# Performance work log

Hardware: AMD Instinct MI355X
Metric: run time of the kernel (lower is better)

Reference implementation:

```python
import jax, jax.numpy as jnp
import numpy as np

D_MODEL = 512
STATE = 128
HALF = STATE // 2
SEQ = 4096
BATCH = 8


def setup_inputs() -> dict:
    key = jax.random.key(0)
    ks = jax.random.split(key, 4)
    u = jax.random.normal(ks[0], (BATCH, SEQ, D_MODEL), dtype=jnp.float32)
    # HiPPO init: Lambda = -0.5 + i*pi*n, n=1..HALF
    n = jnp.arange(1, HALF + 1, dtype=jnp.float32)
    log_Lambda_real = jnp.log(jnp.full((HALF,), 0.5, dtype=jnp.float32))  # log(-real) with real=-0.5
    Lambda_imag = jnp.pi * n
    B_real = jnp.ones((HALF, D_MODEL), dtype=jnp.float32)
    B_imag = jnp.zeros((HALF, D_MODEL), dtype=jnp.float32)
    C_real = jax.random.normal(ks[1], (D_MODEL, HALF), dtype=jnp.float32) / np.sqrt(STATE)
    C_imag = jax.random.normal(ks[2], (D_MODEL, HALF), dtype=jnp.float32) / np.sqrt(STATE)
    D = jax.random.normal(ks[3], (D_MODEL, D_MODEL), dtype=jnp.float32) / np.sqrt(D_MODEL)
    log_Delta = jnp.array([-3.0], dtype=jnp.float32)
    return {
        "u": u,
        "log_Lambda_real": log_Lambda_real,
        "Lambda_imag": Lambda_imag,
        "B_real": B_real,
        "B_imag": B_imag,
        "C_real": C_real,
        "C_imag": C_imag,
        "D": D,
        "log_Delta": log_Delta,
    }


def reference(u, log_Lambda_real, Lambda_imag, B_real, B_imag, C_real, C_imag, D, log_Delta):
    T = u.shape[1]
    Bc = B_real + 1j * B_imag            # (N/2, P) complex
    Cc = C_real + 1j * C_imag            # (P, N/2) complex
    # --- bilinear (Tustin) discretization ---
    Delta = jnp.exp(log_Delta)           # (1,)
    Lambda = -jnp.exp(jnp.clip(log_Lambda_real, -10.0, 10.0)) + 1j * Lambda_imag  # (N/2,)
    denom = 1.0 - (Delta / 2.0) * Lambda
    A_bar = (1.0 + (Delta / 2.0) * Lambda) / denom          # (N/2,)
    B_bar = (Delta / denom)[:, None] * Bc                   # (N/2, P)
    # --- FFT convolution with the SSM kernel k[n,t] = A_bar[n]^t ---
    t_idx = jnp.arange(T)
    k = jnp.exp(jnp.log(A_bar)[:, None] * t_idx[None, :])   # (N/2, T)
    u_c = u.astype(jnp.complex64)
    v = jnp.einsum('np,btp->bnt', B_bar, u_c)               # (B, N/2, T)
    fft_size = 2 * T
    V_f = jnp.fft.fft(v, n=fft_size, axis=-1)
    K_f = jnp.fft.fft(k, n=fft_size, axis=-1)
    conv = jnp.fft.ifft(V_f * K_f[None, :, :], axis=-1)[..., :T]  # (B, N/2, T)
    y = 2.0 * jnp.einsum('pn,bnt->btp', Cc, conv).real      # (B, T, P)
    return y + u @ D.T
```

## Files before the change

kernel.cpp:

```cpp
#include <hip/hip_runtime.h>
#include <hip/hip_bf16.h>
#include <stdint.h>


#define BATCH 8
#define SEQ   4096
#define DMODEL 512
#define HALF  64
#define CHUNK 64
#define NCHUNK (SEQ / CHUNK)

typedef __attribute__((ext_vector_type(8))) short short8;
typedef __attribute__((ext_vector_type(4))) float f32x4;

__device__ __forceinline__ unsigned short f2bf(float f) {
    unsigned int u = __float_as_uint(f);
    u += 0x7fffu + ((u >> 16) & 1u);
    return (unsigned short)(u >> 16);
}

#define GLOAD_LDS16(g, l)                                                    \
    __builtin_amdgcn_global_load_lds(                                        \
        (const __attribute__((address_space(1))) unsigned int*)(g),          \
        (__attribute__((address_space(3))) unsigned int*)(l), 16, 0, 0)


__global__ void k_consts(const float* __restrict__ logLr,
                         const float* __restrict__ Li_in,
                         const float* __restrict__ logDelta,
                         float* __restrict__ sr, float* __restrict__ si,
                         float* __restrict__ ApR, float* __restrict__ ApI) {
    int n = threadIdx.x;
    float Delta = expf(logDelta[0]);
    float llr = fminf(fmaxf(logLr[n], -10.f), 10.f);
    float Lr = -expf(llr);
    float Li = Li_in[n];
    float dr = 1.f - 0.5f * Delta * Lr;
    float di = -0.5f * Delta * Li;
    float dn = dr * dr + di * di;
    float nr = 1.f + 0.5f * Delta * Lr;
    float ni = 0.5f * Delta * Li;
    float Ar = (nr * dr + ni * di) / dn;
    float Ai = (ni * dr - nr * di) / dn;
    sr[n] = Delta * dr / dn;
    si[n] = -Delta * di / dn;
    float pr = 1.f, pi = 0.f;
    for (int k = 0; k <= CHUNK; ++k) {
        ApR[k * HALF + n] = pr;
        ApI[k * HALF + n] = pi;
        float npr = pr * Ar - pi * Ai;
        float npi = pr * Ai + pi * Ar;
        pr = npr; pi = npi;
    }
}

__global__ void k_build_Mv(const float* __restrict__ Br, const float* __restrict__ Bi,
                           const float* __restrict__ sr, const float* __restrict__ si,
                           unsigned short* __restrict__ Mv) {
    int np = blockIdx.x, p = threadIdx.x;
    int n = np & 63;
    float br = Br[n * DMODEL + p], bi = Bi[n * DMODEL + p];
    float v = (np < HALF) ? (sr[n] * br - si[n] * bi)
                          : (si[n] * br + sr[n] * bi);
    Mv[np * DMODEL + p] = f2bf(v);
}

__global__ void k_build_W(const float* __restrict__ Cr, const float* __restrict__ Ci,
                          const float* __restrict__ D, unsigned short* __restrict__ W) {
    int p = blockIdx.x, j = threadIdx.x;
    float v;
    if (j < HALF) v = 2.f * Cr[p * HALF + j];
    else if (j < 2 * HALF) v = -2.f * Ci[p * HALF + (j - HALF)];
    else v = D[p * DMODEL + (j - 2 * HALF)];
    W[p * 640 + j] = f2bf(v);
}


__global__ void k_scanA(const float* __restrict__ V,
                        const float* __restrict__ ApR, const float* __restrict__ ApI,
                        float* __restrict__ E) {
    int tid = threadIdx.x;
    int n = tid & 63;
    int c = ((blockIdx.x & 31) << 1) + (tid >> 6);
    int b = blockIdx.x >> 5;
    float Ar = ApR[HALF + n], Ai = ApI[HALF + n];
    float xr = 0.f, xi = 0.f;
    size_t base = ((size_t)b * SEQ + (size_t)c * CHUNK) * 128 + n;
    for (int tl = 0; tl < CHUNK; ++tl) {
        float vr = V[base], vi = V[base + 64];
        float nxr = Ar * xr - Ai * xi + vr;
        float nxi = Ar * xi + Ai * xr + vi;
        xr = nxr; xi = nxi;
        base += 128;
    }
    int eidx = ((b * NCHUNK + c) * 2) * HALF + n;
    E[eidx] = xr; E[eidx + 64] = xi;
}

__global__ void k_scanB(const float* __restrict__ E, float* __restrict__ Carry,
                        const float* __restrict__ ApR, const float* __restrict__ ApI) {
    int lane = threadIdx.x & 63;
    int wv = threadIdx.x >> 6;
    int b = blockIdx.x;
    for (int n = wv; n < HALF; n += 8) {
        float wr = ApR[CHUNK * HALF + n], wi = ApI[CHUNK * HALF + n];
        int idx = ((b * NCHUNK + lane) * 2) * HALF + n;
        float sR = E[idx], sI = E[idx + 64];
#pragma unroll
        for (int s = 1; s < 64; s <<= 1) {
            float pR = __shfl_up(sR, s, 64);
            float pI = __shfl_up(sI, s, 64);
            if (lane >= s) {
                sR += wr * pR - wi * pI;
                sI += wr * pI + wi * pR;
            }
            float nwr = wr * wr - wi * wi;
            float nwi = 2.f * wr * wi;
            wr = nwr; wi = nwi;
        }
        float cR = __shfl_up(sR, 1, 64);
        float cI = __shfl_up(sI, 1, 64);
        if (lane == 0) { cR = 0.f; cI = 0.f; }
        Carry[idx] = cR; Carry[idx + 64] = cI;
    }
}

template <int WRITE_V, int WRITE_XB>
__global__ void k_scanC(float* __restrict__ V, const float* __restrict__ Carry,
                        const float* __restrict__ ApR, const float* __restrict__ ApI,
                        unsigned short* __restrict__ Xb) {
    int tid = threadIdx.x;
    int n = tid & 63;
    int c = ((blockIdx.x & 31) << 1) + (tid >> 6);
    int b = blockIdx.x >> 5;
    int cidx = ((b * NCHUNK + c) * 2) * HALF + n;
    float xr = Carry[cidx], xi = Carry[cidx + 64];
    float Ar = ApR[HALF + n], Ai = ApI[HALF + n];
    size_t base = ((size_t)b * SEQ + (size_t)c * CHUNK) * 128 + n;
    for (int tl = 0; tl < CHUNK; ++tl) {
        float vr = V[base], vi = V[base + 64];
        float nxr = Ar * xr - Ai * xi + vr;
        float nxi = Ar * xi + Ai * xr + vi;
        xr = nxr; xi = nxi;
        if (WRITE_XB) { Xb[base] = f2bf(xr); Xb[base + 64] = f2bf(xi); }
        if (WRITE_V)  { V[base] = xr; V[base + 64] = xi; }
        base += 128;
    }
}

__global__ __launch_bounds__(512) void gemm1(const float* __restrict__ U,
                                             const unsigned short* __restrict__ Mv,
                                             float* __restrict__ V,
                                             unsigned short* __restrict__ Ub,
                                             int writeUb) {
    __shared__ __align__(16) unsigned short As[64 * 32];
    __shared__ __align__(16) unsigned short Bs[128 * 32];
    const int tid = threadIdx.x;
    const int lane = tid & 63;
    const int w = tid >> 6;
    const int wm = w >> 2, wn = w & 3;
    const int l15 = lane & 15, l4 = lane >> 4;
    const int row0 = blockIdx.x * 64;
    const int srow = tid >> 3;
    const int sh = (tid & 7) * 4;

    f32x4 acc[2][2];
#pragma unroll
    for (int m = 0; m < 2; ++m)
#pragma unroll
        for (int n = 0; n < 2; ++n) acc[m][n] = (f32x4)(0.f);

    for (int k0 = 0; k0 < DMODEL; k0 += 32) {
        const float4 av = *(const float4*)(U + (size_t)(row0 + srow) * DMODEL + k0 + sh);

        __syncthreads();

        GLOAD_LDS16(Mv + (size_t)(tid >> 2) * DMODEL + k0 + (tid & 3) * 8,
                    &Bs[(w * 64) * 8]);

        uint2 wa;
        wa.x = (unsigned)f2bf(av.x) | ((unsigned)f2bf(av.y) << 16);
        wa.y = (unsigned)f2bf(av.z) | ((unsigned)f2bf(av.w) << 16);
        *(uint2*)&As[srow * 32 + sh] = wa;
        if (writeUb)
            *(uint2*)&Ub[(size_t)(row0 + srow) * DMODEL + k0 + sh] = wa;

        __syncthreads();

        short8 af[2], bf[2];
#pragma unroll
        for (int m = 0; m < 2; ++m)
            af[m] = *(const short8*)&As[(wm * 32 + m * 16 + l15) * 32 + l4 * 8];
#pragma unroll
        for (int n = 0; n < 2; ++n)
            bf[n] = *(const short8*)&Bs[(wn * 32 + n * 16 + l15) * 32 + l4 * 8];
#pragma unroll
        for (int m = 0; m < 2; ++m)
#pragma unroll
            for (int n = 0; n < 2; ++n)
                acc[m][n] = __builtin_amdgcn_mfma_f32_16x16x32_bf16(af[m], bf[n], acc[m][n], 0, 0, 0);
    }

#pragma unroll
    for (int m = 0; m < 2; ++m) {
        int rbase = row0 + wm * 32 + m * 16 + l4 * 4;
#pragma unroll
        for (int n = 0; n < 2; ++n) {
            int col = wn * 32 + n * 16 + l15;
#pragma unroll
            for (int r = 0; r < 4; ++r)
                V[(size_t)(rbase + r) * 128 + col] = acc[m][n][r];
        }
    }
}


#define STAGE_A8(t, q) do {                                                    \
    int c_ = (q) * 512 + tid;                                                  \
    int ct_ = c_ ^ (((c_ >> 5) & 1) << 1);                                     \
    int r_ = (ct_ >> 2) & 255;                                                 \
    int kcol_ = (t) * 64 + (ct_ >> 10) * 32 + (ct_ & 3) * 8;                   \
    const unsigned short* src_ = (kcol_ < 128)                                 \
        ? Xb + (size_t)(row0 + r_) * 128 + kcol_                               \
        : Ub + (size_t)(row0 + r_) * 512 + (kcol_ - 128);                      \
    GLOAD_LDS16(src_, &As[((t) & 1) * 16384 + ((q) * 512 + w * 64) * 8]);      \
} while (0)

#define STAGE_B8(t, q) do {                                                    \
    int c_ = (q) * 512 + tid;                                                  \
    int ct_ = c_ ^ (((c_ >> 5) & 1) << 1);                                     \
    int r_ = (ct_ >> 2) & 255;                                                 \
    int kcol_ = (t) * 64 + (ct_ >> 10) * 32 + (ct_ & 3) * 8;                   \
    GLOAD_LDS16(W + (size_t)(col0 + r_) * 640 + kcol_,                         \
                &Bs[((t) & 1) * 16384 + ((q) * 512 + w * 64) * 8]);            \
} while (0)

#define LDA8(t, mq) do {                                                       \
    _Pragma("unroll") for (int m2_ = 0; m2_ < 4; ++m2_)                        \
    _Pragma("unroll") for (int kh_ = 0; kh_ < 2; ++kh_) {                      \
        int r_ = wm * 128 + ((mq) * 4 + m2_) * 16 + l15;                       \
        int c_ = (l4 * 8) ^ (((r_ >> 3) & 1) << 4);                            \
        af[m2_][kh_] = *(const short8*)                                        \
            &As[((t) & 1) * 16384 + kh_ * 8192 + r_ * 32 + c_];                \
    } } while (0)

#define LDB8(t, nq) do {                                                       \
    _Pragma("unroll") for (int n2_ = 0; n2_ < 2; ++n2_)                        \
    _Pragma("unroll") for (int kh_ = 0; kh_ < 2; ++kh_) {                      \
        int r_ = wn * 64 + ((nq) * 2 + n2_) * 16 + l15;                        \
        int c_ = (l4 * 8) ^ (((r_ >> 3) & 1) << 4);                            \
        bf[n2_][kh_] = *(const short8*)                                        \
            &Bs[((t) & 1) * 16384 + kh_ * 8192 + r_ * 32 + c_];                \
    } } while (0)

#define MFMA8(mq, nq) do {                                                     \
    __builtin_amdgcn_s_setprio(1);                                             \
    _Pragma("unroll") for (int m2_ = 0; m2_ < 4; ++m2_)                        \
    _Pragma("unroll") for (int n2_ = 0; n2_ < 2; ++n2_)                        \
    _Pragma("unroll") for (int kh_ = 0; kh_ < 2; ++kh_)                        \
        acc[(mq) * 4 + m2_][(nq) * 2 + n2_] =                                  \
            __builtin_amdgcn_mfma_f32_16x16x32_bf16(                           \
                af[m2_][kh_], bf[n2_][kh_],                                    \
                acc[(mq) * 4 + m2_][(nq) * 2 + n2_], 0, 0, 0);                 \
    __builtin_amdgcn_s_setprio(0);                                             \
} while (0)

__global__ __launch_bounds__(512) void gemm23_8p(const unsigned short* __restrict__ Xb,
                                                 const unsigned short* __restrict__ Ub,
                                                 const unsigned short* __restrict__ W,
                                                 float* __restrict__ C) {
    __shared__ __align__(16) unsigned short As[2 * 16384];
    __shared__ __align__(16) unsigned short Bs[2 * 16384];
    const int tid = threadIdx.x;
    const int lane = tid & 63;
    const int w = tid >> 6;
    const int wm = w >> 2, wn = w & 3;
    const int l15 = lane & 15, l4 = lane >> 4;

    int lin = blockIdx.y * gridDim.x + blockIdx.x;
    int sw = (lin & 7) * 32 + (lin >> 3);
    const int row0 = (sw & 127) * 256;
    const int col0 = (sw >> 7) * 256;

    f32x4 acc[8][4];
#pragma unroll
    for (int m = 0; m < 8; ++m)
#pragma unroll
        for (int n = 0; n < 4; ++n) acc[m][n] = (f32x4)(0.f);

#pragma unroll
    for (int q = 0; q < 4; ++q) { STAGE_A8(0, q); STAGE_B8(0, q); }
    __syncthreads();

    short8 af[4][2], bf[2][2];
    for (int t = 0; t < 10; ++t) {
        const bool pf = (t < 9);
        LDA8(t, 0); LDB8(t, 0);
        if (pf) { STAGE_A8(t + 1, 0); STAGE_B8(t + 1, 0); }
        __builtin_amdgcn_s_barrier();
        MFMA8(0, 0);
        __builtin_amdgcn_s_barrier();
        LDB8(t, 1);
        if (pf) { STAGE_A8(t + 1, 1); STAGE_B8(t + 1, 1); }
        __builtin_amdgcn_s_barrier();
        MFMA8(0, 1);
        __builtin_amdgcn_s_barrier();
        LDA8(t, 1); LDB8(t, 0);
        if (pf) { STAGE_A8(t + 1, 2); STAGE_B8(t + 1, 2); }
        __builtin_amdgcn_s_barrier();
        MFMA8(1, 0);
        __builtin_amdgcn_s_barrier();
        LDB8(t, 1);
        if (pf) { STAGE_A8(t + 1, 3); STAGE_B8(t + 1, 3); }
        __builtin_amdgcn_s_barrier();
        MFMA8(1, 1);
        __syncthreads();
    }

#pragma unroll
    for (int m = 0; m < 8; ++m) {
        int rbase = row0 + wm * 128 + m * 16 + l4 * 4;
#pragma unroll
        for (int n = 0; n < 4; ++n) {
            int col = col0 + wn * 64 + n * 16 + l15;
#pragma unroll
            for (int r = 0; r < 4; ++r)
                C[(size_t)(rbase + r) * DMODEL + col] = acc[m][n][r];
        }
    }
}

__global__ __launch_bounds__(256) void gemm23_f32a(
    const float* __restrict__ A0, int lda0,
    const float* __restrict__ A1, int lda1,
    const unsigned short* __restrict__ B, int ldb,
    float* __restrict__ C, int ldc, int K, int SPLIT)
{
    __shared__ __align__(16) unsigned short As[128 * 32];
    __shared__ __align__(16) unsigned short Bs[128 * 32];
    const int tid = threadIdx.x;
    const int lane = tid & 63;
    const int w = tid >> 6;
    const int wm = w >> 1, wn = w & 1;
    const int l15 = lane & 15, l4 = lane >> 4;
    const int row0 = blockIdx.x * 128;
    const int col0 = blockIdx.y * 128;
    const int srow = tid >> 1;
    const int sh = (tid & 1) << 4;

    f32x4 acc[4][4];
#pragma unroll
    for (int m = 0; m < 4; ++m)
#pragma unroll
        for (int n = 0; n < 4; ++n) acc[m][n] = (f32x4)(0.f);

    for (int k0 = 0; k0 < K; k0 += 32) {
        const float* ap; int lda, kk;
        if (k0 < SPLIT) { ap = A0; lda = lda0; kk = k0; }
        else { ap = A1; lda = lda1; kk = k0 - SPLIT; }
        const float* ag = ap + (size_t)(row0 + srow) * lda + kk + sh;
        float4 av0 = ((const float4*)ag)[0];
        float4 av1 = ((const float4*)ag)[1];
        float4 av2 = ((const float4*)ag)[2];
        float4 av3 = ((const float4*)ag)[3];

        __syncthreads();

#pragma unroll
        for (int i = 0; i < 2; ++i) {
            int c = i * 256 + w * 64 + lane;
            GLOAD_LDS16(B + (size_t)(col0 + (c >> 2)) * ldb + k0 + (c & 3) * 8,
                        &Bs[(i * 256 + w * 64) * 8]);
        }

        uint4 wa0, wa1;
        wa0.x = (unsigned)f2bf(av0.x) | ((unsigned)f2bf(av0.y) << 16);
        wa0.y = (unsigned)f2bf(av0.z) | ((unsigned)f2bf(av0.w) << 16);
        wa0.z = (unsigned)f2bf(av1.x) | ((unsigned)f2bf(av1.y) << 16);
        wa0.w = (unsigned)f2bf(av1.z) | ((unsigned)f2bf(av1.w) << 16);
        wa1.x = (unsigned)f2bf(av2.x) | ((unsigned)f2bf(av2.y) << 16);
        wa1.y = (unsigned)f2bf(av2.z) | ((unsigned)f2bf(av2.w) << 16);
        wa1.z = (unsigned)f2bf(av3.x) | ((unsigned)f2bf(av3.y) << 16);
        wa1.w = (unsigned)f2bf(av3.z) | ((unsigned)f2bf(av3.w) << 16);
        uint4* adst = (uint4*)&As[srow * 32 + sh];
        adst[0] = wa0; adst[1] = wa1;

        __syncthreads();

        short8 af[4], bf[4];
#pragma unroll
        for (int m = 0; m < 4; ++m)
            af[m] = *(const short8*)&As[(wm * 64 + m * 16 + l15) * 32 + l4 * 8];
#pragma unroll
        for (int n = 0; n < 4; ++n)
            bf[n] = *(const short8*)&Bs[(wn * 64 + n * 16 + l15) * 32 + l4 * 8];
#pragma unroll
        for (int m = 0; m < 4; ++m)
#pragma unroll
            for (int n = 0; n < 4; ++n)
                acc[m][n] = __builtin_amdgcn_mfma_f32_16x16x32_bf16(af[m], bf[n], acc[m][n], 0, 0, 0);
    }

#pragma unroll
    for (int m = 0; m < 4; ++m) {
        int rbase = row0 + wm * 64 + m * 16 + l4 * 4;
#pragma unroll
        for (int n = 0; n < 4; ++n) {
            int col = col0 + wn * 64 + n * 16 + l15;
#pragma unroll
            for (int r = 0; r < 4; ++r)
                C[(size_t)(rbase + r) * ldc + col] = acc[m][n][r];
        }
    }
}


extern "C" void kernel_launch(void* const* d_in, const int* in_sizes, int n_in,
                              void* d_out, int out_size, void* d_ws, size_t ws_size,
                              hipStream_t stream) {
    const float* u      = (const float*)d_in[0];
    const float* logLr  = (const float*)d_in[1];
    const float* Li     = (const float*)d_in[2];
    const float* Br     = (const float*)d_in[3];
    const float* Bi     = (const float*)d_in[4];
    const float* Cr     = (const float*)d_in[5];
    const float* Ci     = (const float*)d_in[6];
    const float* D      = (const float*)d_in[7];
    const float* logDel = (const float*)d_in[8];
    float* out = (float*)d_out;

    const size_t M = (size_t)BATCH * SEQ;
    float* ws    = (float*)d_ws;
    float* V     = ws;
    float* E     = V + M * 128;
    float* Carry = E + 65536;
    float* ApR   = Carry + 65536;
    float* ApI   = ApR + 4160;
    float* sr    = ApI + 4160;
    float* si    = sr + 64;
    unsigned short* Mv = (unsigned short*)(si + 64);
    unsigned short* W  = Mv + 128 * 512;
    unsigned short* Ub = W + 512 * 640;
    unsigned short* Xb = Ub + M * 512;
    const size_t need = (size_t)((char*)(Xb + M * 128) - (char*)ws);
    const int big = (ws_size >= need);

    hipLaunchKernelGGL(k_consts, dim3(1), dim3(64), 0, stream,
                       logLr, Li, logDel, sr, si, ApR, ApI);
    hipLaunchKernelGGL(k_build_Mv, dim3(128), dim3(512), 0, stream, Br, Bi, sr, si, Mv);
    hipLaunchKernelGGL(k_build_W, dim3(512), dim3(640), 0, stream, Cr, Ci, D, W);

    hipLaunchKernelGGL(gemm1, dim3(M / 64), dim3(512), 0, stream, u, Mv, V, Ub, big);

    hipLaunchKernelGGL(k_scanA, dim3(256), dim3(128), 0, stream, V, ApR, ApI, E);
    hipLaunchKernelGGL(k_scanB, dim3(BATCH), dim3(512), 0, stream, E, Carry, ApR, ApI);
    if (big) {
        hipLaunchKernelGGL((k_scanC<0, 1>), dim3(256), dim3(128), 0, stream,
                           V, Carry, ApR, ApI, Xb);
        hipLaunchKernelGGL(gemm23_8p, dim3(M / 256, DMODEL / 256), dim3(512), 0, stream,
                           Xb, Ub, W, out);
    } else {
        hipLaunchKernelGGL((k_scanC<1, 0>), dim3(256), dim3(128), 0, stream,
                           V, Carry, ApR, ApI, (unsigned short*)nullptr);
        hipLaunchKernelGGL(gemm23_f32a, dim3(M / 128, DMODEL / 128), dim3(256), 0, stream,
                           V, 128, u, DMODEL, W, 640, out, DMODEL, 640, 128);
    }
}
```

Measured before the change: 89.37 us.

## Store V in bf16, preload Mv into LDS, restructure gemm23 pipeline, drop fallback

Writes the intermediate V in bf16 instead of fp32, halving the traffic of the gemm1 output and of the scan reads. gemm1 now keeps the whole Mv matrix in LDS with an XOR swizzle, uses 128-row tiles and reads U straight into registers. The gemm23 loop moves from four sub-phases to two k-halves with explicit vmcnt waits so loads overlap the MFMAs. The small-workspace fallback path is removed, so a large workspace is assumed, and rounding V to bf16 before the scan adds precision loss.

```diff
diff --git a/kernel.cpp b/kernel.cpp
--- a/kernel.cpp
+++ b/kernel.cpp
@@ -9,6 +9,7 @@
 #define HALF  64
 #define CHUNK 64
 #define NCHUNK (SEQ / CHUNK)
+#define NT    10
 
 typedef __attribute__((ext_vector_type(8))) short short8;
 typedef __attribute__((ext_vector_type(4))) float f32x4;
@@ -17,6 +18,9 @@
     unsigned int u = __float_as_uint(f);
     u += 0x7fffu + ((u >> 16) & 1u);
     return (unsigned short)(u >> 16);
+}
+__device__ __forceinline__ float bf2f(unsigned short s) {
+    return __uint_as_float((unsigned)s << 16);
 }
 
 #define GLOAD_LDS16(g, l)                                                    \
@@ -76,7 +80,7 @@
 }
 
 
-__global__ void k_scanA(const float* __restrict__ V,
+__global__ void k_scanA(const unsigned short* __restrict__ Vb,
                         const float* __restrict__ ApR, const float* __restrict__ ApI,
                         float* __restrict__ E) {
     int tid = threadIdx.x;
@@ -87,7 +91,7 @@
     float xr = 0.f, xi = 0.f;
     size_t base = ((size_t)b * SEQ + (size_t)c * CHUNK) * 128 + n;
     for (int tl = 0; tl < CHUNK; ++tl) {
-        float vr = V[base], vi = V[base + 64];
+        float vr = bf2f(Vb[base]), vi = bf2f(Vb[base + 64]);
         float nxr = Ar * xr - Ai * xi + vr;
         float nxi = Ar * xi + Ai * xr + vi;
         xr = nxr; xi = nxi;
@@ -125,8 +129,8 @@
     }
 }
 
-template <int WRITE_V, int WRITE_XB>
-__global__ void k_scanC(float* __restrict__ V, const float* __restrict__ Carry,
+__global__ void k_scanC(const unsigned short* __restrict__ Vb,
+                        const float* __restrict__ Carry,
                         const float* __restrict__ ApR, const float* __restrict__ ApI,
                         unsigned short* __restrict__ Xb) {
     int tid = threadIdx.x;
@@ -138,130 +142,122 @@
     float Ar = ApR[HALF + n], Ai = ApI[HALF + n];
     size_t base = ((size_t)b * SEQ + (size_t)c * CHUNK) * 128 + n;
     for (int tl = 0; tl < CHUNK; ++tl) {
-        float vr = V[base], vi = V[base + 64];
+        float vr = bf2f(Vb[base]), vi = bf2f(Vb[base + 64]);
         float nxr = Ar * xr - Ai * xi + vr;
         float nxi = Ar * xi + Ai * xr + vi;
         xr = nxr; xi = nxi;
-        if (WRITE_XB) { Xb[base] = f2bf(xr); Xb[base + 64] = f2bf(xi); }
-        if (WRITE_V)  { V[base] = xr; V[base + 64] = xi; }
+        Xb[base] = f2bf(xr); Xb[base + 64] = f2bf(xi);
         base += 128;
     }
 }
 
 __global__ __launch_bounds__(512) void gemm1(const float* __restrict__ U,
                                              const unsigned short* __restrict__ Mv,
-                                             float* __restrict__ V,
-                                             unsigned short* __restrict__ Ub,
-                                             int writeUb) {
-    __shared__ __align__(16) unsigned short As[64 * 32];
-    __shared__ __align__(16) unsigned short Bs[128 * 32];
+                                             unsigned short* __restrict__ Vb,
+                                             unsigned short* __restrict__ Ub) {
+    __shared__ __align__(16) unsigned short Bs[128 * 512];
     const int tid = threadIdx.x;
     const int lane = tid & 63;
     const int w = tid >> 6;
-    const int wm = w >> 2, wn = w & 3;
+    const int wm = w >> 1, wn = w & 1;
     const int l15 = lane & 15, l4 = lane >> 4;
-    const int row0 = blockIdx.x * 64;
-    const int srow = tid >> 3;
-    const int sh = (tid & 7) * 4;
-
-    f32x4 acc[2][2];
-#pragma unroll
-    for (int m = 0; m < 2; ++m)
-#pragma unroll
-        for (int n = 0; n < 2; ++n) acc[m][n] = (f32x4)(0.f);
-
+    const int row0 = blockIdx.x * 128;
+
+#pragma unroll
+    for (int i = 0; i < 16; ++i) {
+        int c = i * 512 + tid;
+        int n = c >> 6;
+        int p = c & 63;
+        int ko = p ^ (n & 7);
+        GLOAD_LDS16(Mv + (size_t)n * DMODEL + ko * 8, &Bs[(i * 512 + w * 64) * 8]);
+    }
+    asm volatile("s_waitcnt vmcnt(0)" ::: "memory");
+    __builtin_amdgcn_s_barrier();
+    __builtin_amdgcn_sched_barrier(0);
+
+    f32x4 acc[2][4];
+#pragma unroll
+    for (int i = 0; i < 2; ++i)
+#pragma unroll
+        for (int j = 0; j < 4; ++j) acc[i][j] = (f32x4)(0.f);
+
+#pragma unroll 2
     for (int k0 = 0; k0 < DMODEL; k0 += 32) {
-        const float4 av = *(const float4*)(U + (size_t)(row0 + srow) * DMODEL + k0 + sh);
-
-        __syncthreads();
-
-        GLOAD_LDS16(Mv + (size_t)(tid >> 2) * DMODEL + k0 + (tid & 3) * 8,
-                    &Bs[(w * 64) * 8]);
-
-        uint2 wa;
-        wa.x = (unsigned)f2bf(av.x) | ((unsigned)f2bf(av.y) << 16);
-        wa.y = (unsigned)f2bf(av.z) | ((unsigned)f2bf(av.w) << 16);
-        *(uint2*)&As[srow * 32 + sh] = wa;
-        if (writeUb)
-            *(uint2*)&Ub[(size_t)(row0 + srow) * DMODEL + k0 + sh] = wa;
-
-        __syncthreads();
-
-        short8 af[2], bf[2];
-#pragma unroll
-        for (int m = 0; m < 2; ++m)
-            af[m] = *(const short8*)&As[(wm * 32 + m * 16 + l15) * 32 + l4 * 8];
-#pragma unroll
-        for (int n = 0; n < 2; ++n)
-            bf[n] = *(const short8*)&Bs[(wn * 32 + n * 16 + l15) * 32 + l4 * 8];
-#pragma unroll
-        for (int m = 0; m < 2; ++m)
-#pragma unroll
-            for (int n = 0; n < 2; ++n)
-                acc[m][n] = __builtin_amdgcn_mfma_f32_16x16x32_bf16(af[m], bf[n], acc[m][n], 0, 0, 0);
-    }
-
-#pragma unroll
-    for (int m = 0; m < 2; ++m) {
-        int rbase = row0 + wm * 32 + m * 16 + l4 * 4;
-#pragma unroll
-        for (int n = 0; n < 2; ++n) {
-            int col = wn * 32 + n * 16 + l15;
+        short8 af[2];
+#pragma unroll
+        for (int i = 0; i < 2; ++i) {
+            int r = row0 + wm * 32 + i * 16 + l15;
+            const float* ag = U + (size_t)r * DMODEL + k0 + l4 * 8;
+            float4 a0 = ((const float4*)ag)[0];
+            float4 a1 = ((const float4*)ag)[1];
+            union { short8 s; uint4 u; } pk;
+            pk.u.x = (unsigned)f2bf(a0.x) | ((unsigned)f2bf(a0.y) << 16);
+            pk.u.y = (unsigned)f2bf(a0.z) | ((unsigned)f2bf(a0.w) << 16);
+            pk.u.z = (unsigned)f2bf(a1.x) | ((unsigned)f2bf(a1.y) << 16);
+            pk.u.w = (unsigned)f2bf(a1.z) | ((unsigned)f2bf(a1.w) << 16);
+            af[i] = pk.s;
+            if (wn == 0)
+                *(uint4*)&Ub[(size_t)r * DMODEL + k0 + l4 * 8] = pk.u;
+        }
+        short8 bf[4];
+#pragma unroll
+        for (int j = 0; j < 4; ++j) {
+            int n = wn * 64 + j * 16 + l15;
+            int q = ((k0 >> 3) + l4) ^ (n & 7);
+            bf[j] = *(const short8*)&Bs[n * DMODEL + q * 8];
+        }
+#pragma unroll
+        for (int i = 0; i < 2; ++i)
+#pragma unroll
+            for (int j = 0; j < 4; ++j)
+                acc[i][j] = __builtin_amdgcn_mfma_f32_16x16x32_bf16(af[i], bf[j], acc[i][j], 0, 0, 0);
+    }
+
+#pragma unroll
+    for (int i = 0; i < 2; ++i) {
+        int rbase = row0 + wm * 32 + i * 16 + l4 * 4;
+#pragma unroll
+        for (int j = 0; j < 4; ++j) {
+            int col = wn * 64 + j * 16 + l15;
 #pragma unroll
             for (int r = 0; r < 4; ++r)
-                V[(size_t)(rbase + r) * 128 + col] = acc[m][n][r];
-        }
-    }
-}
-
-
-#define STAGE_A8(t, q) do {                                                    \
-    int c_ = (q) * 512 + tid;                                                  \
+                Vb[(size_t)(rbase + r) * 128 + col] = f2bf(acc[i][j][r]);
+        }
+    }
+}
+
+
+#define STAGE_K(t, kh, j) do {                                                 \
+    int c_ = (kh) * 1024 + (j) * 512 + tid;                                    \
     int ct_ = c_ ^ (((c_ >> 5) & 1) << 1);                                     \
     int r_ = (ct_ >> 2) & 255;                                                 \
-    int kcol_ = (t) * 64 + (ct_ >> 10) * 32 + (ct_ & 3) * 8;                   \
-    const unsigned short* src_ = (kcol_ < 128)                                 \
+    int kcol_ = (t) * 64 + (kh) * 32 + (ct_ & 3) * 8;                          \
+    const unsigned short* asrc_ = (kcol_ < 128)                                \
         ? Xb + (size_t)(row0 + r_) * 128 + kcol_                               \
         : Ub + (size_t)(row0 + r_) * 512 + (kcol_ - 128);                      \
-    GLOAD_LDS16(src_, &As[((t) & 1) * 16384 + ((q) * 512 + w * 64) * 8]);      \
+    GLOAD_LDS16(asrc_, &As[((t) & 1) * 16384 + ((kh) * 1024 + (j) * 512 + w * 64) * 8]); \
+    GLOAD_LDS16(W + (size_t)(col0 + r_) * 640 + kcol_,                         \
+                &Bs[((t) & 1) * 16384 + ((kh) * 1024 + (j) * 512 + w * 64) * 8]); \
 } while (0)
 
-#define STAGE_B8(t, q) do {                                                    \
-    int c_ = (q) * 512 + tid;                                                  \
-    int ct_ = c_ ^ (((c_ >> 5) & 1) << 1);                                     \
-    int r_ = (ct_ >> 2) & 255;                                                 \
-    int kcol_ = (t) * 64 + (ct_ >> 10) * 32 + (ct_ & 3) * 8;                   \
-    GLOAD_LDS16(W + (size_t)(col0 + r_) * 640 + kcol_,                         \
-                &Bs[((t) & 1) * 16384 + ((q) * 512 + w * 64) * 8]);            \
-} while (0)
-
-#define LDA8(t, mq) do {                                                       \
-    _Pragma("unroll") for (int m2_ = 0; m2_ < 4; ++m2_)                        \
-    _Pragma("unroll") for (int kh_ = 0; kh_ < 2; ++kh_) {                      \
-        int r_ = wm * 128 + ((mq) * 4 + m2_) * 16 + l15;                       \
+#define LDAB(t, kh) do {                                                       \
+    _Pragma("unroll") for (int i_ = 0; i_ < 8; ++i_) {                         \
+        int r_ = wm * 128 + i_ * 16 + l15;                                     \
         int c_ = (l4 * 8) ^ (((r_ >> 3) & 1) << 4);                            \
-        af[m2_][kh_] = *(const short8*)                                        \
-            &As[((t) & 1) * 16384 + kh_ * 8192 + r_ * 32 + c_];                \
+        af[i_] = *(const short8*)&As[((t) & 1) * 16384 + (kh) * 8192 + r_ * 32 + c_]; \
+    }                                                                          \
+    _Pragma("unroll") for (int j_ = 0; j_ < 4; ++j_) {                         \
+        int r_ = wn * 64 + j_ * 16 + l15;                                      \
+        int c_ = (l4 * 8) ^ (((r_ >> 3) & 1) << 4);                            \
+        bf[j_] = *(const short8*)&Bs[((t) & 1) * 16384 + (kh) * 8192 + r_ * 32 + c_]; \
     } } while (0)
 
-#define LDB8(t, nq) do {                                                       \
-    _Pragma("unroll") for (int n2_ = 0; n2_ < 2; ++n2_)                        \
-    _Pragma("unroll") for (int kh_ = 0; kh_ < 2; ++kh_) {                      \
-        int r_ = wn * 64 + ((nq) * 2 + n2_) * 16 + l15;                        \
-        int c_ = (l4 * 8) ^ (((r_ >> 3) & 1) << 4);                            \
-        bf[n2_][kh_] = *(const short8*)                                        \
-            &Bs[((t) & 1) * 16384 + kh_ * 8192 + r_ * 32 + c_];                \
-    } } while (0)
-
-#define MFMA8(mq, nq) do {                                                     \
+#define MFMA32() do {                                                          \
     __builtin_amdgcn_s_setprio(1);                                             \
-    _Pragma("unroll") for (int m2_ = 0; m2_ < 4; ++m2_)                        \
-    _Pragma("unroll") for (int n2_ = 0; n2_ < 2; ++n2_)                        \
-    _Pragma("unroll") for (int kh_ = 0; kh_ < 2; ++kh_)                        \
-        acc[(mq) * 4 + m2_][(nq) * 2 + n2_] =                                  \
-            __builtin_amdgcn_mfma_f32_16x16x32_bf16(                           \
-                af[m2_][kh_], bf[n2_][kh_],                                    \
-                acc[(mq) * 4 + m2_][(nq) * 2 + n2_], 0, 0, 0);                 \
+    _Pragma("unroll") for (int i_ = 0; i_ < 8; ++i_)                           \
+    _Pragma("unroll") for (int j_ = 0; j_ < 4; ++j_)                           \
+        acc[i_][j_] = __builtin_amdgcn_mfma_f32_16x16x32_bf16(                 \
+            af[i_], bf[j_], acc[i_][j_], 0, 0, 0);                             \
     __builtin_amdgcn_s_setprio(0);                                             \
 } while (0)
 
@@ -288,33 +284,32 @@
 #pragma unroll
         for (int n = 0; n < 4; ++n) acc[m][n] = (f32x4)(0.f);
 
-#pragma unroll
-    for (int q = 0; q < 4; ++q) { STAGE_A8(0, q); STAGE_B8(0, q); }
-    __syncthreads();
-
-    short8 af[4][2], bf[2][2];
-    for (int t = 0; t < 10; ++t) {
-        const bool pf = (t < 9);
-        LDA8(t, 0); LDB8(t, 0);
-        if (pf) { STAGE_A8(t + 1, 0); STAGE_B8(t + 1, 0); }
+    STAGE_K(0, 0, 0); STAGE_K(0, 0, 1);
+    STAGE_K(0, 1, 0); STAGE_K(0, 1, 1);
+    asm volatile("s_waitcnt vmcnt(4)" ::: "memory");
+    __builtin_amdgcn_s_barrier();
+    __builtin_amdgcn_sched_barrier(0);
+
+    short8 af[8], bf[4];
+    for (int t = 0; t < NT; ++t) {
+        const bool pf = (t < NT - 1);
+        LDAB(t, 0);
+        if (pf) { STAGE_K(t + 1, 0, 0); STAGE_K(t + 1, 0, 1); }
         __builtin_amdgcn_s_barrier();
-        MFMA8(0, 0);
+        __builtin_amdgcn_sched_barrier(0);
+        MFMA32();
+        if (pf) asm volatile("s_waitcnt vmcnt(4)" ::: "memory");
+        else    asm volatile("s_waitcnt vmcnt(0)" ::: "memory");
         __builtin_amdgcn_s_barrier();
-        LDB8(t, 1);
-        if (pf) { STAGE_A8(t + 1, 1); STAGE_B8(t + 1, 1); }
+        __builtin_amdgcn_sched_barrier(0);
+        LDAB(t, 1);
+        if (pf) { STAGE_K(t + 1, 1, 0); STAGE_K(t + 1, 1, 1); }
         __builtin_amdgcn_s_barrier();
-        MFMA8(0, 1);
+        __builtin_amdgcn_sched_barrier(0);
+        MFMA32();
+        if (pf) asm volatile("s_waitcnt vmcnt(4)" ::: "memory");
         __builtin_amdgcn_s_barrier();
-        LDA8(t, 1); LDB8(t, 0);
-        if (pf) { STAGE_A8(t + 1, 2); STAGE_B8(t + 1, 2); }
-        __builtin_amdgcn_s_barrier();
-        MFMA8(1, 0);
-        __builtin_amdgcn_s_barrier();
-        LDB8(t, 1);
-        if (pf) { STAGE_A8(t + 1, 3); STAGE_B8(t + 1, 3); }
-        __builtin_amdgcn_s_barrier();
-        MFMA8(1, 1);
-        __syncthreads();
+        __builtin_amdgcn_sched_barrier(0);
     }
 
 #pragma unroll
@@ -326,90 +321,6 @@
 #pragma unroll
             for (int r = 0; r < 4; ++r)
                 C[(size_t)(rbase + r) * DMODEL + col] = acc[m][n][r];
-        }
-    }
-}
-
-__global__ __launch_bounds__(256) void gemm23_f32a(
-    const float* __restrict__ A0, int lda0,
-    const float* __restrict__ A1, int lda1,
-    const unsigned short* __restrict__ B, int ldb,
-    float* __restrict__ C, int ldc, int K, int SPLIT)
-{
-    __shared__ __align__(16) unsigned short As[128 * 32];
-    __shared__ __align__(16) unsigned short Bs[128 * 32];
-    const int tid = threadIdx.x;
-    const int lane = tid & 63;
-    const int w = tid >> 6;
-    const int wm = w >> 1, wn = w & 1;
-    const int l15 = lane & 15, l4 = lane >> 4;
-    const int row0 = blockIdx.x * 128;
-    const int col0 = blockIdx.y * 128;
-    const int srow = tid >> 1;
-    const int sh = (tid & 1) << 4;
-
-    f32x4 acc[4][4];
-#pragma unroll
-    for (int m = 0; m < 4; ++m)
-#pragma unroll
-        for (int n = 0; n < 4; ++n) acc[m][n] = (f32x4)(0.f);
-
-    for (int k0 = 0; k0 < K; k0 += 32) {
-        const float* ap; int lda, kk;
-        if (k0 < SPLIT) { ap = A0; lda = lda0; kk = k0; }
-        else { ap = A1; lda = lda1; kk = k0 - SPLIT; }
-        const float* ag = ap + (size_t)(row0 + srow) * lda + kk + sh;
-        float4 av0 = ((const float4*)ag)[0];
-        float4 av1 = ((const float4*)ag)[1];
-        float4 av2 = ((const float4*)ag)[2];
-        float4 av3 = ((const float4*)ag)[3];
-
-        __syncthreads();
-
-#pragma unroll
-        for (int i = 0; i < 2; ++i) {
-            int c = i * 256 + w * 64 + lane;
-            GLOAD_LDS16(B + (size_t)(col0 + (c >> 2)) * ldb + k0 + (c & 3) * 8,
-                        &Bs[(i * 256 + w * 64) * 8]);
-        }
-
-        uint4 wa0, wa1;
-        wa0.x = (unsigned)f2bf(av0.x) | ((unsigned)f2bf(av0.y) << 16);
-        wa0.y = (unsigned)f2bf(av0.z) | ((unsigned)f2bf(av0.w) << 16);
-        wa0.z = (unsigned)f2bf(av1.x) | ((unsigned)f2bf(av1.y) << 16);
-        wa0.w = (unsigned)f2bf(av1.z) | ((unsigned)f2bf(av1.w) << 16);
-        wa1.x = (unsigned)f2bf(av2.x) | ((unsigned)f2bf(av2.y) << 16);
-        wa1.y = (unsigned)f2bf(av2.z) | ((unsigned)f2bf(av2.w) << 16);
-        wa1.z = (unsigned)f2bf(av3.x) | ((unsigned)f2bf(av3.y) << 16);
-        wa1.w = (unsigned)f2bf(av3.z) | ((unsigned)f2bf(av3.w) << 16);
-        uint4* adst = (uint4*)&As[srow * 32 + sh];
-        adst[0] = wa0; adst[1] = wa1;
-
-        __syncthreads();
-
-        short8 af[4], bf[4];
-#pragma unroll
-        for (int m = 0; m < 4; ++m)
-            af[m] = *(const short8*)&As[(wm * 64 + m * 16 + l15) * 32 + l4 * 8];
-#pragma unroll
-        for (int n = 0; n < 4; ++n)
-            bf[n] = *(const short8*)&Bs[(wn * 64 + n * 16 + l15) * 32 + l4 * 8];
-#pragma unroll
-        for (int m = 0; m < 4; ++m)
-#pragma unroll
-            for (int n = 0; n < 4; ++n)
-                acc[m][n] = __builtin_amdgcn_mfma_f32_16x16x32_bf16(af[m], bf[n], acc[m][n], 0, 0, 0);
-    }
-
-#pragma unroll
-    for (int m = 0; m < 4; ++m) {
-        int rbase = row0 + wm * 64 + m * 16 + l4 * 4;
-#pragma unroll
-        for (int n = 0; n < 4; ++n) {
-            int col = col0 + wn * 64 + n * 16 + l15;
-#pragma unroll
-            for (int r = 0; r < 4; ++r)
-                C[(size_t)(rbase + r) * ldc + col] = acc[m][n][r];
         }
     }
 }
@@ -430,39 +341,30 @@
     float* out = (float*)d_out;
 
     const size_t M = (size_t)BATCH * SEQ;
-    float* ws    = (float*)d_ws;
-    float* V     = ws;
-    float* E     = V + M * 128;
+    unsigned short* Vb = (unsigned short*)d_ws;
+    unsigned short* Ub = Vb + M * 128;
+    unsigned short* Xb = Ub + M * 512;
+    unsigned short* Mv = Xb + M * 128;
+    unsigned short* W  = Mv + 128 * 512;
+    float* fp    = (float*)(W + 512 * 640);
+    float* E     = fp;
     float* Carry = E + 65536;
     float* ApR   = Carry + 65536;
     float* ApI   = ApR + 4160;
     float* sr    = ApI + 4160;
     float* si    = sr + 64;
-    unsigned short* Mv = (unsigned short*)(si + 64);
-    unsigned short* W  = Mv + 128 * 512;
-    unsigned short* Ub = W + 512 * 640;
-    unsigned short* Xb = Ub + M * 512;
-    const size_t need = (size_t)((char*)(Xb + M * 128) - (char*)ws);
-    const int big = (ws_size >= need);
 
     hipLaunchKernelGGL(k_consts, dim3(1), dim3(64), 0, stream,
                        logLr, Li, logDel, sr, si, ApR, ApI);
     hipLaunchKernelGGL(k_build_Mv, dim3(128), dim3(512), 0, stream, Br, Bi, sr, si, Mv);
     hipLaunchKernelGGL(k_build_W, dim3(512), dim3(640), 0, stream, Cr, Ci, D, W);
 
-    hipLaunchKernelGGL(gemm1, dim3(M / 64), dim3(512), 0, stream, u, Mv, V, Ub, big);
-
-    hipLaunchKernelGGL(k_scanA, dim3(256), dim3(128), 0, stream, V, ApR, ApI, E);
+    hipLaunchKernelGGL(gemm1, dim3(M / 128), dim3(512), 0, stream, u, Mv, Vb, Ub);
+
+    hipLaunchKernelGGL(k_scanA, dim3(256), dim3(128), 0, stream, Vb, ApR, ApI, E);
     hipLaunchKernelGGL(k_scanB, dim3(BATCH), dim3(512), 0, stream, E, Carry, ApR, ApI);
-    if (big) {
-        hipLaunchKernelGGL((k_scanC<0, 1>), dim3(256), dim3(128), 0, stream,
-                           V, Carry, ApR, ApI, Xb);
-        hipLaunchKernelGGL(gemm23_8p, dim3(M / 256, DMODEL / 256), dim3(512), 0, stream,
-                           Xb, Ub, W, out);
-    } else {
-        hipLaunchKernelGGL((k_scanC<1, 0>), dim3(256), dim3(128), 0, stream,
-                           V, Carry, ApR, ApI, (unsigned short*)nullptr);
-        hipLaunchKernelGGL(gemm23_f32a, dim3(M / 128, DMODEL / 128), dim3(256), 0, stream,
-                           V, 128, u, DMODEL, W, 640, out, DMODEL, 640, 128);
-    }
-}
+    hipLaunchKernelGGL(k_scanC, dim3(256), dim3(128), 0, stream, Vb, Carry, ApR, ApI, Xb);
+
+    hipLaunchKernelGGL(gemm23_8p, dim3(M / 256, DMODEL / 256), dim3(512), 0, stream,
+                       Xb, Ub, W, out);
+}
```

Result: slower. 92.52 us (+3.5%).
